# Optimization experiments

Measured on AMD Instinct MI355X. Metric: run time of the kernel, lower is better.

## Reference

```python
import jax, jax.numpy as jnp
import numpy as np

B, H, S, D = 8, 16, 1024, 64

def setup_inputs() -> dict:
    key = jax.random.key(0)
    k1, k2, k3, k4 = jax.random.split(key, 4)
    Q = jax.random.normal(k1, (B, H, S, D), dtype=jnp.float32)
    K = jax.random.normal(k2, (B, H, S, D), dtype=jnp.float32)
    V = jax.random.normal(k3, (B, H, S, D), dtype=jnp.float32)
    mask = jax.random.randint(k4, (B,), 0, 2).astype(jnp.bool_)
    return {"Q": Q, "K": K, "V": V, "mask": mask}

def reference(Q, K, V, mask):
    # scores: [B,H,S,S]
    scores = jnp.einsum('bhqd,bhkd->bhqk', Q, K)
    # per-batch-element mask broadcast over heads and both seq dims
    scores = jnp.where(mask[:, None, None, None], jnp.float32(-1e9), scores)
    # NOTE: original divides by sqrt(d) AFTER masking, so masked value is -1e9/sqrt(d)
    inv_sqrt_d = jnp.float32(1.0 / np.sqrt(Q.shape[-1]))
    attn = jax.nn.softmax(scores * inv_sqrt_d, axis=-1)
    return jnp.einsum('bhqk,bhkd->bhqd', attn, V)
```

## Files before the change

kernel.cpp:

```cpp
#include <hip/hip_runtime.h>
#include <hip/hip_bf16.h>

typedef __bf16 bf16;
typedef __bf16 bf16x4 __attribute__((ext_vector_type(4)));
typedef __bf16 bf16x8 __attribute__((ext_vector_type(8)));
typedef float  f32x16 __attribute__((ext_vector_type(16)));

#define S_  1024
#define D_  64
#define BQ  256
#define BK  64
#define KT  (S_/BK)
#define QT  (S_/BQ)
#define LD  72

#define ZERO16 {0.f,0.f,0.f,0.f,0.f,0.f,0.f,0.f,0.f,0.f,0.f,0.f,0.f,0.f,0.f,0.f}

__global__ __launch_bounds__(256, 2)
void fa_fwd(const float* __restrict__ Q, const float* __restrict__ K,
            const float* __restrict__ V, const int* __restrict__ mask,
            float* __restrict__ O)
{
    __shared__ bf16 ks[2][BK][LD];
    __shared__ bf16 vt[2][D_][LD];

    const int tid  = threadIdx.x;
    const int lane = tid & 63;
    const int w    = tid >> 6;
    const int l32  = lane & 31;
    const int hi   = lane >> 5;

    const int bid   = blockIdx.x;
    const int xcd   = bid & 7;
    const int rnd   = bid >> 3;
    const int qtile = rnd & 3;
    const int bh    = ((rnd >> 2) << 3) | xcd;
    const int b     = bh >> 4;
    const size_t base = (size_t)bh * (S_ * D_);
    const int qW = qtile * BQ + w * 64;

    const float qscale = (mask[b] != 0) ? 0.0f : 0.1803368801111204f;

    bf16x8 qf[2][4];
    #pragma unroll
    for (int nt = 0; nt < 2; ++nt) {
        const float* qp = Q + base + (size_t)(qW + nt * 32 + l32) * D_ + hi * 8;
        #pragma unroll
        for (int kc = 0; kc < 4; ++kc) {
            float4 a = *(const float4*)(qp + kc * 16);
            float4 c = *(const float4*)(qp + kc * 16 + 4);
            bf16x8 f;
            f[0] = (bf16)(a.x * qscale); f[1] = (bf16)(a.y * qscale);
            f[2] = (bf16)(a.z * qscale); f[3] = (bf16)(a.w * qscale);
            f[4] = (bf16)(c.x * qscale); f[5] = (bf16)(c.y * qscale);
            f[6] = (bf16)(c.z * qscale); f[7] = (bf16)(c.w * qscale);
            qf[nt][kc] = f;
        }
    }

    f32x16 o[2][2];
    #pragma unroll
    for (int dm = 0; dm < 2; ++dm)
        #pragma unroll
        for (int nt = 0; nt < 2; ++nt) o[dm][nt] = (f32x16)ZERO16;
    float lsum[2] = {0.f, 0.f};

    const int vkq = (tid >> 2) & 15;
    const int vkp = (vkq & 12) | ((vkq & 1) << 1) | ((vkq >> 1) & 1);
    const int vc4 = (tid & 3) + 4 * w;
    const float4* gk = (const float4*)(K + base);
    const float4* gv = (const float4*)(V + base);

    float4 kr[4], vr[4];
    #pragma unroll
    for (int it = 0; it < 4; ++it) kr[it] = gk[it * 256 + tid];
    #pragma unroll
    for (int r = 0; r < 4; ++r)    vr[r]  = gv[(vkq * 4 + r) * 16 + vc4];

    auto mkpf = [&](const f32x16& sv, bf16x8& fA, bf16x8& fB, float& ls) {
        bf16x8 a, c;
        #pragma unroll
        for (int i = 0; i < 8; ++i) {
            float e0 = __builtin_amdgcn_exp2f(sv[i]);
            float e1 = __builtin_amdgcn_exp2f(sv[8 + i]);
            ls += e0 + e1;
            a[i] = (bf16)e0;
            c[i] = (bf16)e1;
        }
        fA = a; fB = c;
    };

    for (int kt = 0; kt < KT; ++kt) {
        bf16 (*ksb)[LD] = ks[kt & 1];
        bf16 (*vtb)[LD] = vt[kt & 1];

        #pragma unroll
        for (int it = 0; it < 4; ++it) {
            int i = it * 256 + tid;
            int row = i >> 4, c4 = i & 15;
            bf16x4 hk = {(bf16)kr[it].x, (bf16)kr[it].y, (bf16)kr[it].z, (bf16)kr[it].w};
            *(bf16x4*)&ksb[row][c4 * 4] = hk;
        }
        {
            bf16x4 t0 = {(bf16)vr[0].x, (bf16)vr[1].x, (bf16)vr[2].x, (bf16)vr[3].x};
            bf16x4 t1 = {(bf16)vr[0].y, (bf16)vr[1].y, (bf16)vr[2].y, (bf16)vr[3].y};
            bf16x4 t2 = {(bf16)vr[0].z, (bf16)vr[1].z, (bf16)vr[2].z, (bf16)vr[3].z};
            bf16x4 t3 = {(bf16)vr[0].w, (bf16)vr[1].w, (bf16)vr[2].w, (bf16)vr[3].w};
            *(bf16x4*)&vtb[vc4 * 4 + 0][vkp * 4] = t0;
            *(bf16x4*)&vtb[vc4 * 4 + 1][vkp * 4] = t1;
            *(bf16x4*)&vtb[vc4 * 4 + 2][vkp * 4] = t2;
            *(bf16x4*)&vtb[vc4 * 4 + 3][vkp * 4] = t3;
        }
        {
            int ktn = (kt + 1 < KT) ? (kt + 1) : kt;
            #pragma unroll
            for (int it = 0; it < 4; ++it) kr[it] = gk[ktn * 1024 + it * 256 + tid];
            #pragma unroll
            for (int r = 0; r < 4; ++r)    vr[r]  = gv[ktn * 1024 + (vkq * 4 + r) * 16 + vc4];
        }
        __syncthreads();

        f32x16 s00 = ZERO16, s01 = ZERO16, s10 = ZERO16, s11 = ZERO16;
        #pragma unroll
        for (int kc = 0; kc < 4; ++kc) {
            bf16x8 k0 = *(const bf16x8*)&ksb[l32][kc * 16 + hi * 8];
            bf16x8 k1 = *(const bf16x8*)&ksb[32 + l32][kc * 16 + hi * 8];
            s00 = __builtin_amdgcn_mfma_f32_32x32x16_bf16(k0, qf[0][kc], s00, 0, 0, 0);
            s01 = __builtin_amdgcn_mfma_f32_32x32x16_bf16(k0, qf[1][kc], s01, 0, 0, 0);
            s10 = __builtin_amdgcn_mfma_f32_32x32x16_bf16(k1, qf[0][kc], s10, 0, 0, 0);
            s11 = __builtin_amdgcn_mfma_f32_32x32x16_bf16(k1, qf[1][kc], s11, 0, 0, 0);
        }

        bf16x8 pf[4][2];
        mkpf(s00, pf[0][0], pf[1][0], lsum[0]);
        mkpf(s01, pf[0][1], pf[1][1], lsum[1]);
        mkpf(s10, pf[2][0], pf[3][0], lsum[0]);
        mkpf(s11, pf[2][1], pf[3][1], lsum[1]);

        #pragma unroll
        for (int kc = 0; kc < 4; ++kc) {
            bf16x8 v0 = *(const bf16x8*)&vtb[l32][kc * 16 + hi * 8];
            bf16x8 v1 = *(const bf16x8*)&vtb[32 + l32][kc * 16 + hi * 8];
            o[0][0] = __builtin_amdgcn_mfma_f32_32x32x16_bf16(v0, pf[kc][0], o[0][0], 0, 0, 0);
            o[0][1] = __builtin_amdgcn_mfma_f32_32x32x16_bf16(v0, pf[kc][1], o[0][1], 0, 0, 0);
            o[1][0] = __builtin_amdgcn_mfma_f32_32x32x16_bf16(v1, pf[kc][0], o[1][0], 0, 0, 0);
            o[1][1] = __builtin_amdgcn_mfma_f32_32x32x16_bf16(v1, pf[kc][1], o[1][1], 0, 0, 0);
        }
    }

    #pragma unroll
    for (int nt = 0; nt < 2; ++nt) {
        float lv = lsum[nt] + __shfl_xor(lsum[nt], 32);
        float inv = 1.0f / lv;
        float* op = O + base + (size_t)(qW + nt * 32 + l32) * D_ + hi * 4;
        #pragma unroll
        for (int g = 0; g < 4; ++g) {
            float4 a = { o[0][nt][g * 4 + 0] * inv, o[0][nt][g * 4 + 1] * inv,
                         o[0][nt][g * 4 + 2] * inv, o[0][nt][g * 4 + 3] * inv };
            *(float4*)(op + g * 8) = a;
            float4 c = { o[1][nt][g * 4 + 0] * inv, o[1][nt][g * 4 + 1] * inv,
                         o[1][nt][g * 4 + 2] * inv, o[1][nt][g * 4 + 3] * inv };
            *(float4*)(op + 32 + g * 8) = c;
        }
    }
}

extern "C" void kernel_launch(void* const* d_in, const int* in_sizes, int n_in,
                              void* d_out, int out_size, void* d_ws, size_t ws_size,
                              hipStream_t stream)
{
    const float* Q    = (const float*)d_in[0];
    const float* K    = (const float*)d_in[1];
    const float* V    = (const float*)d_in[2];
    const int*   mask = (const int*)d_in[3];
    float*       O    = (float*)d_out;

    dim3 grid(8 * 16 * QT);
    fa_fwd<<<grid, 256, 0, stream>>>(Q, K, V, mask, O);
}
```

Before: 150.5 us.

## Deepen K/V register prefetch to two tiles ahead with a manually unrolled loop

Global K/V loads are now issued two tiles ahead into two alternating register sets, with the main loop unrolled by two so each half stages into a fixed LDS buffer. The first two tile loads are issued before the Q loads to overlap startup latency. __syncthreads is replaced by an inline-asm lgkmcnt wait plus s_barrier, which avoids waiting on outstanding global loads (vmcnt) at the barrier. This costs another 32 VGPRs of prefetch registers, which may pressure occupancy under launch bounds of 2 blocks per SIMD.

```diff
diff --git a/kernel.cpp b/kernel.cpp
--- a/kernel.cpp
+++ b/kernel.cpp
@@ -41,6 +41,24 @@
 
     const float qscale = (mask[b] != 0) ? 0.0f : 0.1803368801111204f;
 
+    const int vkq = (tid >> 2) & 15;
+    const int vkp = (vkq & 12) | ((vkq & 1) << 1) | ((vkq >> 1) & 1);
+    const int vc4 = (tid & 3) + 4 * w;
+    const float4* gk = (const float4*)(K + base);
+    const float4* gv = (const float4*)(V + base);
+
+    float4 krA[4], vrA[4], krB[4], vrB[4];
+
+    auto issue = [&](float4* krp, float4* vrp, int t) {
+        #pragma unroll
+        for (int it = 0; it < 4; ++it) krp[it] = gk[t * 1024 + it * 256 + tid];
+        #pragma unroll
+        for (int r = 0; r < 4; ++r)    vrp[r]  = gv[t * 1024 + (vkq * 4 + r) * 16 + vc4];
+    };
+
+    issue(krA, vrA, 0);
+    issue(krB, vrB, 1);
+
     bf16x8 qf[2][4];
     #pragma unroll
     for (int nt = 0; nt < 2; ++nt) {
@@ -65,17 +83,25 @@
         for (int nt = 0; nt < 2; ++nt) o[dm][nt] = (f32x16)ZERO16;
     float lsum[2] = {0.f, 0.f};
 
-    const int vkq = (tid >> 2) & 15;
-    const int vkp = (vkq & 12) | ((vkq & 1) << 1) | ((vkq >> 1) & 1);
-    const int vc4 = (tid & 3) + 4 * w;
-    const float4* gk = (const float4*)(K + base);
-    const float4* gv = (const float4*)(V + base);
-
-    float4 kr[4], vr[4];
-    #pragma unroll
-    for (int it = 0; it < 4; ++it) kr[it] = gk[it * 256 + tid];
-    #pragma unroll
-    for (int r = 0; r < 4; ++r)    vr[r]  = gv[(vkq * 4 + r) * 16 + vc4];
+    auto stage = [&](const float4* krp, const float4* vrp, int buf) {
+        bf16 (*ksb)[LD] = ks[buf];
+        bf16 (*vtb)[LD] = vt[buf];
+        #pragma unroll
+        for (int it = 0; it < 4; ++it) {
+            int i = it * 256 + tid;
+            int row = i >> 4, c4 = i & 15;
+            bf16x4 hk = {(bf16)krp[it].x, (bf16)krp[it].y, (bf16)krp[it].z, (bf16)krp[it].w};
+            *(bf16x4*)&ksb[row][c4 * 4] = hk;
+        }
+        bf16x4 t0 = {(bf16)vrp[0].x, (bf16)vrp[1].x, (bf16)vrp[2].x, (bf16)vrp[3].x};
+        bf16x4 t1 = {(bf16)vrp[0].y, (bf16)vrp[1].y, (bf16)vrp[2].y, (bf16)vrp[3].y};
+        bf16x4 t2 = {(bf16)vrp[0].z, (bf16)vrp[1].z, (bf16)vrp[2].z, (bf16)vrp[3].z};
+        bf16x4 t3 = {(bf16)vrp[0].w, (bf16)vrp[1].w, (bf16)vrp[2].w, (bf16)vrp[3].w};
+        *(bf16x4*)&vtb[vc4 * 4 + 0][vkp * 4] = t0;
+        *(bf16x4*)&vtb[vc4 * 4 + 1][vkp * 4] = t1;
+        *(bf16x4*)&vtb[vc4 * 4 + 2][vkp * 4] = t2;
+        *(bf16x4*)&vtb[vc4 * 4 + 3][vkp * 4] = t3;
+    };
 
     auto mkpf = [&](const f32x16& sv, bf16x8& fA, bf16x8& fB, float& ls) {
         bf16x8 a, c;
@@ -90,35 +116,9 @@
         fA = a; fB = c;
     };
 
-    for (int kt = 0; kt < KT; ++kt) {
-        bf16 (*ksb)[LD] = ks[kt & 1];
-        bf16 (*vtb)[LD] = vt[kt & 1];
-
-        #pragma unroll
-        for (int it = 0; it < 4; ++it) {
-            int i = it * 256 + tid;
-            int row = i >> 4, c4 = i & 15;
-            bf16x4 hk = {(bf16)kr[it].x, (bf16)kr[it].y, (bf16)kr[it].z, (bf16)kr[it].w};
-            *(bf16x4*)&ksb[row][c4 * 4] = hk;
-        }
-        {
-            bf16x4 t0 = {(bf16)vr[0].x, (bf16)vr[1].x, (bf16)vr[2].x, (bf16)vr[3].x};
-            bf16x4 t1 = {(bf16)vr[0].y, (bf16)vr[1].y, (bf16)vr[2].y, (bf16)vr[3].y};
-            bf16x4 t2 = {(bf16)vr[0].z, (bf16)vr[1].z, (bf16)vr[2].z, (bf16)vr[3].z};
-            bf16x4 t3 = {(bf16)vr[0].w, (bf16)vr[1].w, (bf16)vr[2].w, (bf16)vr[3].w};
-            *(bf16x4*)&vtb[vc4 * 4 + 0][vkp * 4] = t0;
-            *(bf16x4*)&vtb[vc4 * 4 + 1][vkp * 4] = t1;
-            *(bf16x4*)&vtb[vc4 * 4 + 2][vkp * 4] = t2;
-            *(bf16x4*)&vtb[vc4 * 4 + 3][vkp * 4] = t3;
-        }
-        {
-            int ktn = (kt + 1 < KT) ? (kt + 1) : kt;
-            #pragma unroll
-            for (int it = 0; it < 4; ++it) kr[it] = gk[ktn * 1024 + it * 256 + tid];
-            #pragma unroll
-            for (int r = 0; r < 4; ++r)    vr[r]  = gv[ktn * 1024 + (vkq * 4 + r) * 16 + vc4];
-        }
-        __syncthreads();
+    auto compute = [&](int buf) {
+        bf16 (*ksb)[LD] = ks[buf];
+        bf16 (*vtb)[LD] = vt[buf];
 
         f32x16 s00 = ZERO16, s01 = ZERO16, s10 = ZERO16, s11 = ZERO16;
         #pragma unroll
@@ -146,6 +146,20 @@
             o[1][0] = __builtin_amdgcn_mfma_f32_32x32x16_bf16(v1, pf[kc][0], o[1][0], 0, 0, 0);
             o[1][1] = __builtin_amdgcn_mfma_f32_32x32x16_bf16(v1, pf[kc][1], o[1][1], 0, 0, 0);
         }
+    };
+
+#define BARRIER() asm volatile("s_waitcnt lgkmcnt(0)\n\ts_barrier" ::: "memory")
+
+    #pragma unroll 1
+    for (int kt = 0; kt < KT; kt += 2) {
+        stage(krA, vrA, 0);
+        if (kt + 2 < KT) issue(krA, vrA, kt + 2);
+        BARRIER();
+        compute(0);
+        stage(krB, vrB, 1);
+        if (kt + 3 < KT) issue(krB, vrB, kt + 3);
+        BARRIER();
+        compute(1);
     }
 
     #pragma unroll
```

Measured after the change: 175.9 us. +16.9%, slower.

## Route masked batches to a cheap mean-of-V path and compact heavy blocks

Applied to the files above, without the earlier changes.

Each block reads the mask for all batches and assigns blocks so that the full attention work covers only unmasked batches. Masked batches get a light path: one block per head that averages V over the sequence and broadcasts that mean to every output row. A masked row has uniform softmax, so the mean is exact. This skips the QK and PV matmuls for masked batches, at the cost of per-block mask scanning, some idle early-exit blocks, and a single-block-per-head light path that may become a tail.

```diff
diff --git a/kernel.cpp b/kernel.cpp
--- a/kernel.cpp
+++ b/kernel.cpp
@@ -29,17 +29,84 @@
     const int w    = tid >> 6;
     const int l32  = lane & 31;
     const int hi   = lane >> 5;
-
-    const int bid   = blockIdx.x;
-    const int xcd   = bid & 7;
-    const int rnd   = bid >> 3;
-    const int qtile = rnd & 3;
-    const int bh    = ((rnd >> 2) << 3) | xcd;
-    const int b     = bh >> 4;
+    const int bid  = blockIdx.x;
+
+    int m0 = mask[0], m1 = mask[1], m2 = mask[2], m3 = mask[3];
+    int m4 = mask[4], m5 = mask[5], m6 = mask[6], m7 = mask[7];
+    int um[8] = { m0 == 0, m1 == 0, m2 == 0, m3 == 0,
+                  m4 == 0, m5 == 0, m6 == 0, m7 == 0 };
+    int U = 0;
+    #pragma unroll
+    for (int i = 0; i < 8; ++i) U += um[i];
+    const int nHeavy = 64 * U;
+    const int nLight = 16 * (8 - U);
+
+    int bh, qtile;
+    bool light;
+    if (bid < nHeavy) {
+        const int xcd = bid & 7;
+        const int r   = bid >> 3;
+        qtile = r & 3;
+        const int g   = r >> 2;
+        const int bh_rank = (g << 3) | xcd;
+        const int ub   = bh_rank >> 4;
+        const int head = bh_rank & 15;
+        int b = 0, cnt = 0;
+        #pragma unroll
+        for (int i = 0; i < 8; ++i) { if (um[i]) { if (cnt == ub) b = i; ++cnt; } }
+        bh = b * 16 + head;
+        light = false;
+    } else if (bid < nHeavy + nLight) {
+        const int lid    = bid - nHeavy;
+        const int m_rank = lid >> 4;
+        const int head   = lid & 15;
+        int b = 0, cnt = 0;
+        #pragma unroll
+        for (int i = 0; i < 8; ++i) { if (!um[i]) { if (cnt == m_rank) b = i; ++cnt; } }
+        bh = b * 16 + head;
+        qtile = 0;
+        light = true;
+    } else {
+        return;
+    }
+
     const size_t base = (size_t)bh * (S_ * D_);
+
+    if (light) {
+        const float4* gvl = (const float4*)(V + base);
+        float4*       gol = (float4*)(O + base);
+        const int d4 = tid & 15;
+        const int rg = tid >> 4;
+        float4 acc = {0.f, 0.f, 0.f, 0.f};
+        #pragma unroll 4
+        for (int r = 0; r < 64; ++r) {
+            float4 v = gvl[(rg * 64 + r) * 16 + d4];
+            acc.x += v.x; acc.y += v.y; acc.z += v.z; acc.w += v.w;
+        }
+        float4 (*red)[16] = (float4(*)[16])&ks[0][0][0];
+        red[rg][d4] = acc;
+        __syncthreads();
+        if (tid < 16) {
+            float4 s = red[0][tid];
+            #pragma unroll
+            for (int g = 1; g < 16; ++g) {
+                float4 t = red[g][tid];
+                s.x += t.x; s.y += t.y; s.z += t.z; s.w += t.w;
+            }
+            const float sc = 1.0f / 1024.0f;
+            s.x *= sc; s.y *= sc; s.z *= sc; s.w *= sc;
+            red[0][tid] = s;
+        }
+        __syncthreads();
+        float4 mv = red[0][d4];
+        #pragma unroll 4
+        for (int k = 0; k < 64; ++k)
+            gol[(rg + 16 * k) * 16 + d4] = mv;
+        return;
+    }
+
     const int qW = qtile * BQ + w * 64;
-
-    const float qscale = (mask[b] != 0) ? 0.0f : 0.1803368801111204f;
+    const float qscale = 0.1803368801111204f;
 
     bf16x8 qf[2][4];
     #pragma unroll
```

Measured after the change: 136.7 us. -9.2%, faster.
